# Performance work log

Hardware: AMD Instinct MI355X
Metric: run time of the kernel (lower is better)

Reference implementation:

```python
import jax, jax.numpy as jnp
import numpy as np

# ---- module constants (from init_kwargs) ----
NOF_LINKS = 64
NOISE = 1e-3          # gen_para.input_noise_power
DT = 0.01             # gen_para.dt
T_END = 5.12          # t
TXP = 1.0             # gen_para.tx_power
LAM = 1.0
RHO = 1.0

T_ARR = jnp.arange(0.0, T_END, DT, dtype=jnp.float32)   # [T] time grid
POW2T = jnp.power(jnp.float32(2.0), T_ARR)               # 2^t
POW2T_1 = POW2T - 1.0                                    # 2^t - 1
LN2 = jnp.log(jnp.float32(2.0))


def setup_inputs() -> dict:
    key = jax.random.key(0)
    k1, k2 = jax.random.split(key)
    pathloss = jax.random.uniform(k1, (NOF_LINKS, NOF_LINKS), dtype=jnp.float32)
    powers = jax.random.uniform(k2, (16, 20, NOF_LINKS), dtype=jnp.float32)
    return {"pathloss": pathloss, "powers": powers}


def _outage(pathloss, power):
    # power: [B, N, L]; pathloss: [L, L]
    B, N, L = power.shape
    T = T_ARR.shape[0]
    # signal[b,n,i,j] = pathloss[i,j] * power[b,n,i]  (per original expand/permute)
    y_ii = jnp.diagonal(pathloss)[None, None, :] * power              # [B,N,L]
    y_tot = power * jnp.sum(pathloss, axis=1)[None, None, :]          # sum_j signal
    y_ij = y_tot - y_ii
    sinr = y_ii / (y_ij + NOISE)                                      # [B,N,L]

    # block-0 outage CDF over time grid: Q1[b,i,t] = 1 - exp(-(2^t-1) * sinr[b,0,i])
    Q1 = 1.0 - jnp.exp(-POW2T_1[None, None, :] * sinr[:, 0, :, None])  # [B,L,T]

    # per-block pdf kernels for n >= 1 (vectorized over all blocks up front)
    s = sinr[:, 1:, :, None]                                          # [B,N-1,L,1]
    q = jnp.exp(-POW2T_1 * s) * POW2T * s * LN2                       # [B,N-1,L,T]

    def step(Q, qn):
        # Q, qn: [B,L,T]; per-channel grouped cross-correlation (torch conv1d semantics)
        x = Q.reshape(1, B * L, T)
        w = qn.reshape(B * L, 1, T)
        out = jax.lax.conv_general_dilated(
            x, w, window_strides=(1,), padding=[(T - 1, T - 1)],
            feature_group_count=B * L)                                 # [1,B*L,2T-1]
        Qn = out[0, :, :T].reshape(B, L, T) * DT
        return Qn, Qn[:, :, -1]

    q_scan = jnp.moveaxis(q, 1, 0)                                    # [N-1,B,L,T]
    _, outa_rest = jax.lax.scan(step, Q1, q_scan)                     # [N-1,B,L]
    outa = jnp.concatenate([Q1[None, :, :, -1], outa_rest], axis=0)   # [N,B,L]
    return jnp.moveaxis(outa, 0, 1)                                   # [B,N,L]


def reference(pathloss, powers):
    power = powers * TXP
    N = power.shape[1]
    outa = _outage(pathloss, power)                                   # [B,N,L]
    E = power[:, 0, :] + jnp.sum(power[:, 1:, :] * outa[:, :N - 1, :], axis=1)
    D = 1.0 + jnp.sum(outa[:, :N - 1, :], axis=1)
    loss = jnp.sum(E) + LAM * jnp.sum(outa[:, N - 1, :]) + RHO * jnp.sum(D)
    return loss
```

## Files before the change

kernel.cpp:

```cpp
#include <hip/hip_runtime.h>

#define LL 64
#define NN 20
#define DTC 0.01f
#define NOISEC 1e-3f
#define LN2C 0.69314718056f

typedef __attribute__((ext_vector_type(8))) short short8x;
typedef __attribute__((ext_vector_type(4))) float f32x4;
typedef __attribute__((ext_vector_type(4))) int v4i;

__device__ __forceinline__ unsigned bf16r(float x) {
    union { float f; unsigned u; } a; a.f = x;
    return (a.u + (0x7fffu + ((a.u >> 16) & 1u))) >> 16;
}
__device__ __forceinline__ unsigned pk_bf16(float x, float y) {
    return bf16r(x) | (bf16r(y) << 16);
}

template<int CTRL>
__device__ __forceinline__ short8x dpp_shr(short8x v) {
    v4i p = __builtin_bit_cast(v4i, v);
    v4i q;
    q.x = __builtin_amdgcn_update_dpp(0, p.x, CTRL, 0xf, 0xf, true);
    q.y = __builtin_amdgcn_update_dpp(0, p.y, CTRL, 0xf, 0xf, true);
    q.z = __builtin_amdgcn_update_dpp(0, p.z, CTRL, 0xf, 0xf, true);
    q.w = __builtin_amdgcn_update_dpp(0, p.w, CTRL, 0xf, 0xf, true);
    return __builtin_bit_cast(short8x, q);
}

__device__ __forceinline__ short8x derive_m16(short8x dNext, short8x dCur, bool hi32) {
    v4i a = __builtin_bit_cast(v4i, dNext);
    v4i b = __builtin_bit_cast(v4i, dCur);
    v4i r;
    { auto s = __builtin_amdgcn_permlane32_swap(a.x, b.x, false, false); r.x = hi32 ? s[0] : s[1]; }
    { auto s = __builtin_amdgcn_permlane32_swap(a.y, b.y, false, false); r.y = hi32 ? s[0] : s[1]; }
    { auto s = __builtin_amdgcn_permlane32_swap(a.z, b.z, false, false); r.z = hi32 ? s[0] : s[1]; }
    { auto s = __builtin_amdgcn_permlane32_swap(a.w, b.w, false, false); r.w = hi32 ? s[0] : s[1]; }
    return __builtin_bit_cast(short8x, r);
}

__global__ __launch_bounds__(64, 1) void outage_kernel(
    const float* __restrict__ pathloss,
    const float* __restrict__ powers,
    float* __restrict__ out)
{
    __shared__ __align__(16) unsigned short gt[2][8][544];
    __shared__ __align__(16) unsigned short Qb[2][1024];

    const int lane = threadIdx.x;
    const int c = blockIdx.x, b = c >> 6, l = c & 63;
    const int nh = lane & 15;
    const int qd = lane >> 4;
    const bool hi32 = (lane >= 32);

    const float pl = pathloss[l * LL + lane];
    float rs = pl;
    #pragma unroll
    for (int mk = 1; mk < 64; mk <<= 1) rs += __shfl_xor(rs, mk, 64);
    const float dg   = __shfl(pl, l, 64);
    const float dsum = rs - dg;

    float P2[8], P1[8];
    #pragma unroll
    for (int u = 0; u < 8; ++u) {
        P2[u] = exp2f((8 * lane + u) * DTC);
        P1[u] = P2[u] - 1.f;
    }

    *((uint4*)&Qb[0][0] + lane) = uint4{0u, 0u, 0u, 0u};
    *((uint4*)&Qb[1][0] + lane) = uint4{0u, 0u, 0u, 0u};
    {
        const int bb = lane >> 5, w = lane & 31;
        #pragma unroll
        for (int k = 0; k < 8; ++k) gt[bb][k][512 + w] = 0;
    }

    const float p0 = powers[(b * NN + 0) * LL + l];
    const float s0 = dg * p0 / (p0 * dsum + NOISEC);
    float q7;
    {
        float v[8];
        #pragma unroll
        for (int u = 0; u < 8; ++u) v[u] = 1.f - expf(-P1[u] * s0);
        q7 = v[7];
        uint4 d4 = { pk_bf16(v[0], v[1]), pk_bf16(v[2], v[3]),
                     pk_bf16(v[4], v[5]), pk_bf16(v[6], v[7]) };
        *(uint4*)&Qb[0][512 + 8 * lane] = d4;
    }

    const float p1v = powers[(b * NN + 1) * LL + l];
    float lossCh = 1.f + p0 + (p1v + 1.f) * q7;

    auto fill_g = [&](int buf, float p) {
        float s  = dg * p / (p * dsum + NOISEC);
        float cm = s * LN2C * DTC;
        unsigned F[8];
        #pragma unroll
        for (int w = 0; w < 4; ++w) {
            float a  = expf(-P1[2 * w] * s) * P2[2 * w] * cm;
            float bb = expf(-P1[2 * w + 1] * s) * P2[2 * w + 1] * cm;
            F[w] = pk_bf16(a, bb);
        }
        #pragma unroll
        for (int w = 0; w < 4; ++w) {
            unsigned t = (unsigned)__shfl_down((int)F[w], 1, 64);
            F[4 + w] = (lane == 63) ? 0u : t;
        }
        unsigned E[7];
        #pragma unroll
        for (int j = 0; j < 7; ++j) E[j] = (F[j] >> 16) | (F[j + 1] << 16);
        #pragma unroll
        for (int k = 0; k < 8; ++k) {
            uint4 d4;
            if ((k & 1) == 0) d4 = uint4{F[k / 2], F[k / 2 + 1], F[k / 2 + 2], F[k / 2 + 3]};
            else              d4 = uint4{E[k / 2], E[k / 2 + 1], E[k / 2 + 2], E[k / 2 + 3]};
            *(uint4*)&gt[buf][k][8 * lane] = d4;
        }
    };
    fill_g(1, p1v);

    const int kk    = (7 - nh) & 7;
    const int baseA = 511 - nh + 8 * qd - kk;
    const int baseB = 512 + 32 * nh + 8 * qd;
    const int dstw  = 512 + 32 * nh + 4 * qd;

    float pnext = powers[(b * NN + 2) * LL + l];

    for (int n = 1; n < NN; ++n) {
        const unsigned short* psrc = &Qb[(n + 1) & 1][0];
        const unsigned short* pg   = &gt[n & 1][kk][0];
        unsigned short* pdst       = &Qb[n & 1][0];

        float pfut = 0.f;
        if (n <= NN - 3) pfut = powers[(b * NN + n + 2) * LL + l];

        short8x Bv[16];
        Bv[0]  = *(const short8x*)&psrc[baseB];
        Bv[1]  = dpp_shr<0x111>(Bv[0]);
        Bv[2]  = dpp_shr<0x112>(Bv[0]);
        Bv[3]  = dpp_shr<0x113>(Bv[0]);
        Bv[4]  = dpp_shr<0x114>(Bv[0]);
        Bv[5]  = dpp_shr<0x115>(Bv[0]);
        Bv[6]  = dpp_shr<0x116>(Bv[0]);
        Bv[7]  = dpp_shr<0x117>(Bv[0]);
        Bv[8]  = dpp_shr<0x118>(Bv[0]);
        Bv[9]  = dpp_shr<0x119>(Bv[0]);
        Bv[10] = dpp_shr<0x11A>(Bv[0]);
        Bv[11] = dpp_shr<0x11B>(Bv[0]);
        Bv[12] = dpp_shr<0x11C>(Bv[0]);
        Bv[13] = dpp_shr<0x11D>(Bv[0]);
        Bv[14] = dpp_shr<0x11E>(Bv[0]);
        Bv[15] = dpp_shr<0x11F>(Bv[0]);

        short8x A0v[16];
        #pragma unroll
        for (int d = 0; d < 16; ++d) A0v[d] = *(const short8x*)&pg[baseA - 32 * d];
        const short8x A15 = *(const short8x*)&pg[baseA - 32 * 15 - 16];

        if (n < NN - 1) fill_g((n + 1) & 1, pnext);

        f32x4 acc0a = {0.f, 0.f, 0.f, 0.f}, acc0b = {0.f, 0.f, 0.f, 0.f};
        f32x4 acc1a = {0.f, 0.f, 0.f, 0.f}, acc1b = {0.f, 0.f, 0.f, 0.f};
        #pragma unroll
        for (int d = 0; d < 16; d += 2) {
            short8x A1e = derive_m16(A0v[d + 1], A0v[d], hi32);
            short8x A1o;
            if (d < 14) A1o = derive_m16(A0v[d + 2], A0v[d + 1], hi32);
            else        A1o = A15;
            acc0a = __builtin_amdgcn_mfma_f32_16x16x32_bf16(A0v[d],     Bv[d],     acc0a, 0, 0, 0);
            acc1a = __builtin_amdgcn_mfma_f32_16x16x32_bf16(A1e,        Bv[d],     acc1a, 0, 0, 0);
            acc0b = __builtin_amdgcn_mfma_f32_16x16x32_bf16(A0v[d + 1], Bv[d + 1], acc0b, 0, 0, 0);
            acc1b = __builtin_amdgcn_mfma_f32_16x16x32_bf16(A1o,        Bv[d + 1], acc1b, 0, 0, 0);
        }
        f32x4 acc0 = acc0a + acc0b;
        f32x4 acc1 = acc1a + acc1b;

        *(uint2*)&pdst[dstw]      = uint2{pk_bf16(acc0.x, acc0.y), pk_bf16(acc0.z, acc0.w)};
        *(uint2*)&pdst[dstw + 16] = uint2{pk_bf16(acc1.x, acc1.y), pk_bf16(acc1.z, acc1.w)};

        float wgt = (n < NN - 1) ? (pnext + 1.f) : 1.f;
        lossCh += wgt * acc1.w;
        pnext = pfut;
    }

    if (lane == 63) atomicAdd(out, lossCh);
}

extern "C" void kernel_launch(void* const* d_in, const int* in_sizes, int n_in,
                              void* d_out, int out_size, void* d_ws, size_t ws_size,
                              hipStream_t stream) {
    const float* pathloss = (const float*)d_in[0];
    const float* powers   = (const float*)d_in[1];
    float* outp = (float*)d_out;

    (void)hipMemsetAsync(d_out, 0, sizeof(float) * out_size, stream);
    outage_kernel<<<16 * LL, 64, 0, stream>>>(pathloss, powers, outp);
}
```

Measured before the change: 99.60 us.

## Use hardware bf16 pack, raw exp2, and direct LDS loads for shifted A operands

Replaces the software round-to-nearest bf16 packing with the v_cvt_pk_bf16_f32 instruction. Swaps expf for the raw hardware exp2 with the log2(e) scale folded into precomputed constants. Replaces the permlane32_swap derivation of the 16-shifted A fragments with 16 extra LDS loads. The aim is fewer VALU and cross-lane ops on the serial per-step path, at the cost of more LDS traffic and registers and slightly different exp accuracy.

```diff
diff --git a/kernel.cpp b/kernel.cpp
--- a/kernel.cpp
+++ b/kernel.cpp
@@ -5,17 +5,16 @@
 #define DTC 0.01f
 #define NOISEC 1e-3f
 #define LN2C 0.69314718056f
+#define LOG2E 1.44269504089f
 
 typedef __attribute__((ext_vector_type(8))) short short8x;
 typedef __attribute__((ext_vector_type(4))) float f32x4;
 typedef __attribute__((ext_vector_type(4))) int v4i;
 
-__device__ __forceinline__ unsigned bf16r(float x) {
-    union { float f; unsigned u; } a; a.f = x;
-    return (a.u + (0x7fffu + ((a.u >> 16) & 1u))) >> 16;
-}
-__device__ __forceinline__ unsigned pk_bf16(float x, float y) {
-    return bf16r(x) | (bf16r(y) << 16);
+__device__ __forceinline__ unsigned cvt_pk_bf16(float x, float y) {
+    unsigned r;
+    asm("v_cvt_pk_bf16_f32 %0, %1, %2" : "=v"(r) : "v"(x), "v"(y));
+    return r;
 }
 
 template<int CTRL>
@@ -27,17 +26,6 @@
     q.z = __builtin_amdgcn_update_dpp(0, p.z, CTRL, 0xf, 0xf, true);
     q.w = __builtin_amdgcn_update_dpp(0, p.w, CTRL, 0xf, 0xf, true);
     return __builtin_bit_cast(short8x, q);
-}
-
-__device__ __forceinline__ short8x derive_m16(short8x dNext, short8x dCur, bool hi32) {
-    v4i a = __builtin_bit_cast(v4i, dNext);
-    v4i b = __builtin_bit_cast(v4i, dCur);
-    v4i r;
-    { auto s = __builtin_amdgcn_permlane32_swap(a.x, b.x, false, false); r.x = hi32 ? s[0] : s[1]; }
-    { auto s = __builtin_amdgcn_permlane32_swap(a.y, b.y, false, false); r.y = hi32 ? s[0] : s[1]; }
-    { auto s = __builtin_amdgcn_permlane32_swap(a.z, b.z, false, false); r.z = hi32 ? s[0] : s[1]; }
-    { auto s = __builtin_amdgcn_permlane32_swap(a.w, b.w, false, false); r.w = hi32 ? s[0] : s[1]; }
-    return __builtin_bit_cast(short8x, r);
 }
 
 __global__ __launch_bounds__(64, 1) void outage_kernel(
@@ -52,7 +40,6 @@
     const int c = blockIdx.x, b = c >> 6, l = c & 63;
     const int nh = lane & 15;
     const int qd = lane >> 4;
-    const bool hi32 = (lane >= 32);
 
     const float pl = pathloss[l * LL + lane];
     float rs = pl;
@@ -61,11 +48,12 @@
     const float dg   = __shfl(pl, l, 64);
     const float dsum = rs - dg;
 
-    float P2[8], P1[8];
+    float P2[8], P1L[8];
     #pragma unroll
     for (int u = 0; u < 8; ++u) {
-        P2[u] = exp2f((8 * lane + u) * DTC);
-        P1[u] = P2[u] - 1.f;
+        float e = __builtin_amdgcn_exp2f((8 * lane + u) * DTC);
+        P2[u]  = e;
+        P1L[u] = (1.f - e) * LOG2E;
     }
 
     *((uint4*)&Qb[0][0] + lane) = uint4{0u, 0u, 0u, 0u};
@@ -82,10 +70,10 @@
     {
         float v[8];
         #pragma unroll
-        for (int u = 0; u < 8; ++u) v[u] = 1.f - expf(-P1[u] * s0);
+        for (int u = 0; u < 8; ++u) v[u] = 1.f - __builtin_amdgcn_exp2f(P1L[u] * s0);
         q7 = v[7];
-        uint4 d4 = { pk_bf16(v[0], v[1]), pk_bf16(v[2], v[3]),
-                     pk_bf16(v[4], v[5]), pk_bf16(v[6], v[7]) };
+        uint4 d4 = { cvt_pk_bf16(v[0], v[1]), cvt_pk_bf16(v[2], v[3]),
+                     cvt_pk_bf16(v[4], v[5]), cvt_pk_bf16(v[6], v[7]) };
         *(uint4*)&Qb[0][512 + 8 * lane] = d4;
     }
 
@@ -98,9 +86,9 @@
         unsigned F[8];
         #pragma unroll
         for (int w = 0; w < 4; ++w) {
-            float a  = expf(-P1[2 * w] * s) * P2[2 * w] * cm;
-            float bb = expf(-P1[2 * w + 1] * s) * P2[2 * w + 1] * cm;
-            F[w] = pk_bf16(a, bb);
+            float a  = __builtin_amdgcn_exp2f(P1L[2 * w]     * s) * (P2[2 * w]     * cm);
+            float bb = __builtin_amdgcn_exp2f(P1L[2 * w + 1] * s) * (P2[2 * w + 1] * cm);
+            F[w] = cvt_pk_bf16(a, bb);
         }
         #pragma unroll
         for (int w = 0; w < 4; ++w) {
@@ -153,10 +141,12 @@
         Bv[14] = dpp_shr<0x11E>(Bv[0]);
         Bv[15] = dpp_shr<0x11F>(Bv[0]);
 
-        short8x A0v[16];
+        short8x A0v[16], A1v[16];
         #pragma unroll
-        for (int d = 0; d < 16; ++d) A0v[d] = *(const short8x*)&pg[baseA - 32 * d];
-        const short8x A15 = *(const short8x*)&pg[baseA - 32 * 15 - 16];
+        for (int d = 0; d < 16; ++d) {
+            A0v[d] = *(const short8x*)&pg[baseA - 32 * d];
+            A1v[d] = *(const short8x*)&pg[baseA - 32 * d - 16];
+        }
 
         if (n < NN - 1) fill_g((n + 1) & 1, pnext);
 
@@ -164,20 +154,16 @@
         f32x4 acc1a = {0.f, 0.f, 0.f, 0.f}, acc1b = {0.f, 0.f, 0.f, 0.f};
         #pragma unroll
         for (int d = 0; d < 16; d += 2) {
-            short8x A1e = derive_m16(A0v[d + 1], A0v[d], hi32);
-            short8x A1o;
-            if (d < 14) A1o = derive_m16(A0v[d + 2], A0v[d + 1], hi32);
-            else        A1o = A15;
             acc0a = __builtin_amdgcn_mfma_f32_16x16x32_bf16(A0v[d],     Bv[d],     acc0a, 0, 0, 0);
-            acc1a = __builtin_amdgcn_mfma_f32_16x16x32_bf16(A1e,        Bv[d],     acc1a, 0, 0, 0);
+            acc1a = __builtin_amdgcn_mfma_f32_16x16x32_bf16(A1v[d],     Bv[d],     acc1a, 0, 0, 0);
             acc0b = __builtin_amdgcn_mfma_f32_16x16x32_bf16(A0v[d + 1], Bv[d + 1], acc0b, 0, 0, 0);
-            acc1b = __builtin_amdgcn_mfma_f32_16x16x32_bf16(A1o,        Bv[d + 1], acc1b, 0, 0, 0);
+            acc1b = __builtin_amdgcn_mfma_f32_16x16x32_bf16(A1v[d + 1], Bv[d + 1], acc1b, 0, 0, 0);
         }
         f32x4 acc0 = acc0a + acc0b;
         f32x4 acc1 = acc1a + acc1b;
 
-        *(uint2*)&pdst[dstw]      = uint2{pk_bf16(acc0.x, acc0.y), pk_bf16(acc0.z, acc0.w)};
-        *(uint2*)&pdst[dstw + 16] = uint2{pk_bf16(acc1.x, acc1.y), pk_bf16(acc1.z, acc1.w)};
+        *(uint2*)&pdst[dstw]      = uint2{cvt_pk_bf16(acc0.x, acc0.y), cvt_pk_bf16(acc0.z, acc0.w)};
+        *(uint2*)&pdst[dstw + 16] = uint2{cvt_pk_bf16(acc1.x, acc1.y), cvt_pk_bf16(acc1.z, acc1.w)};
 
         float wgt = (n < NN - 1) ? (pnext + 1.f) : 1.f;
         lossCh += wgt * acc1.w;
```

After: 85.59 us. 1.16x faster.
